# Kernel optimization log

Hardware: AMD Instinct MI355X
Metric: run time of the kernel (lower is better)

## Reference

```python
import jax, jax.numpy as jnp
import numpy as np

N = 50000   # nodes
E = 800000  # edges (avg degree 16)
IN = 128    # in_dim
R = 4       # rank
CMB = 64    # combine_dim
H = 4       # heads
D = 64      # hidden_dim per head
NEG_SLOPE = 0.2


def setup_inputs() -> dict:
    key = jax.random.key(0)
    ks = iter(jax.random.split(key, 24))
    def rnd(shape, s):
        return jax.random.normal(next(ks), shape, jnp.float32) * s
    src = jax.random.randint(next(ks), (E,), 0, N, jnp.int32)
    dst = jax.random.randint(next(ks), (E,), 0, N, jnp.int32)
    ones = jnp.ones((N, 1), jnp.float32)
    # buffers built in __init__: features with a trailing ones column
    h_common = jnp.concatenate([rnd((N, IN), 1.0), ones], axis=-1)      # (N, 129)
    h_type = jnp.concatenate([rnd((N, 512), 1.0), ones], axis=-1)       # (N, 513)
    h_rel = jnp.concatenate([rnd((N, 512), 1.0), ones], axis=-1)        # (N, 513)
    return {
        'src': src, 'dst': dst,
        'h_common': h_common, 'h_type': h_type, 'h_rel': h_rel,
        'Wc': rnd((R, IN + 1, CMB), 0.05),
        'Wt': rnd((R, 513, CMB), 0.05),
        'Wr': rnd((R, 513, CMB), 0.05),
        'fw': rnd((1, R), 0.5),
        'fb': rnd((1, CMB), 0.1),
        'W0': rnd((CMB, H * D), 0.05),
        'al0': rnd((H, D), 0.05), 'ar0': rnd((H, D), 0.05),
        'b0': rnd((H * D,), 0.05),
        'W1': rnd((H * D, H * D), 0.05),
        'al1': rnd((H, D), 0.05), 'ar1': rnd((H, D), 0.05),
        'b1': rnd((H * D,), 0.05),
    }


def _gat_layer(h, src, dst, W, al, ar, b, residual):
    # h: (N, F_in) -> out: (N, H*D), attention a: (E, H)
    feat = (h @ W).reshape(N, H, D)
    el = jnp.einsum('nhd,hd->nh', feat, al)  # (N, H)
    er = jnp.einsum('nhd,hd->nh', feat, ar)
    e = jax.nn.leaky_relu(el[src] + er[dst], NEG_SLOPE)  # (E, H)
    # edge softmax over incoming edges of each dst node
    m = jax.ops.segment_max(e, dst, num_segments=N)      # (N, H)
    ee = jnp.exp(e - m[dst])
    s = jax.ops.segment_sum(ee, dst, num_segments=N)
    a = ee / s[dst]                                       # (E, H)
    msg = feat[src] * a[:, :, None]                       # (E, H, D)
    out = jax.ops.segment_sum(msg, dst, num_segments=N)   # (N, H, D)
    if residual:
        out = out + h.reshape(N, H, D)
    out = out + b.reshape(1, H, D)
    return out.reshape(N, H * D), a


def reference(src, dst, h_common, h_type, h_rel, Wc, Wt, Wr, fw, fb,
              W0, al0, ar0, b0, W1, al1, ar1, b1):
    # low-rank trilinear fusion
    fc = jnp.einsum('ni,ric->rnc', h_common, Wc)  # (R, N, CMB)
    ft = jnp.einsum('ni,ric->rnc', h_type, Wt)
    fr = jnp.einsum('ni,ric->rnc', h_rel, Wr)
    zy = fc * ft * fr
    h = jnp.einsum('r,rnc->nc', fw[0], zy) + fb   # (N, CMB)
    h = jax.nn.elu(h)
    # stacked GAT layers
    h, att = _gat_layer(h, src, dst, W0, al0, ar0, b0, residual=False)
    h, att = _gat_layer(h, src, dst, W1, al1, ar1, b1, residual=True)
    return h, att
```

## Files before the change

kernel.cpp:

```cpp
#include <hip/hip_runtime.h>
#include <math.h>

#define NN 50000
#define EE 800000
#define NEG 0.2f
#define NG (NN / 16)

using f32x4  = __attribute__((ext_vector_type(4))) float;
using bf16x8 = __attribute__((ext_vector_type(8))) short;

__device__ __forceinline__ float lrelu(float x){ return x > 0.f ? x : NEG*x; }

__device__ __forceinline__ unsigned short f2b(float f){
    unsigned int u = __float_as_uint(f);
    return (unsigned short)((u + 0x7FFFu + ((u >> 16) & 1u)) >> 16);
}
__device__ __forceinline__ float b2f(unsigned short h){
    return __uint_as_float(((unsigned int)h) << 16);
}
__device__ __forceinline__ void gld_lds16(const void* g, void* l){
    __builtin_amdgcn_global_load_lds(
        (const __attribute__((address_space(1))) unsigned int*)g,
        (__attribute__((address_space(3))) unsigned int*)l, 16, 0, 0);
}

__global__ void pack_w_fusion(const float* __restrict__ W, unsigned short* __restrict__ out,
                              int K, int NKC)
{
    int u = blockIdx.x * blockDim.x + threadIdx.x;
    if (u >= NKC * 16 * 64) return;
    int l = u & 63, chunk = (u >> 6) & 15, kc = u >> 10;
    int ct = chunk >> 2, r = chunk & 3;
    int c = ct * 16 + (l & 15);
    int kb = kc * 32 + (l >> 4) * 8;
    bf16x8 v;
#pragma unroll
    for (int j = 0; j < 8; ++j)
        v[j] = (short)f2b(W[((size_t)r * K + kb + j) * 64 + c]);
    *(bf16x8*)(out + (size_t)u * 8) = v;
}

template<int PERM>
__global__ void pack_w_gemm(const float* __restrict__ W, unsigned short* __restrict__ out,
                            int K, int C)
{
    int NCH = C / 16;
    int total = (K / 32) * NCH * 64;
    int u = blockIdx.x * blockDim.x + threadIdx.x;
    if (u >= total) return;
    int l = u & 63, ch = (u >> 6) % NCH, kc = u / (64 * NCH);
    int c = ch * 16 + (l & 15);
    int kb = kc * 32 + (l >> 4) * 8;
    bf16x8 v;
#pragma unroll
    for (int j = 0; j < 8; ++j) {
        int k = kb + j;
        int ko = PERM ? ((k & 3) * 64 + (k >> 2)) : k;
        v[j] = (short)f2b(W[(size_t)ko * C + c]);
    }
    *(bf16x8*)(out + (size_t)u * 8) = v;
}

template<int KT, int NKC>
__global__ __launch_bounds__(256) void pack_a_tile(
    const float* __restrict__ F, unsigned short* __restrict__ out)
{
    constexpr int TILES = NKC / 4;
    __shared__ float sf[16][130];
    const int tid = threadIdx.x;
    const int g = blockIdx.x / TILES, t = blockIdx.x % TILES;
    const int nb = g * 16, k0 = t * 128;

#pragma unroll
    for (int i = 0; i < 8; ++i) {
        int idx = tid + i * 256;
        int row = idx >> 7, k = idx & 127;
        sf[row][k] = F[(size_t)(nb + row) * KT + k0 + k];
    }
    __syncthreads();
    {
        int kcl = tid >> 6, l = tid & 63;
        int row = l & 15, kb = kcl * 32 + (l >> 4) * 8;
        bf16x8 o;
#pragma unroll
        for (int j = 0; j < 8; ++j) o[j] = (short)f2b(sf[row][kb + j]);
        *(bf16x8*)(out + ((size_t)(g * NKC + t * 4 + kcl) * 64 + l) * 8) = o;
    }
}

template<int NKC>
__device__ __forceinline__ void fusion_pass_lds(
    const unsigned short* __restrict__ ldsA, int cbase,
    const unsigned short* __restrict__ wp,
    const float* __restrict__ W, int K, int w, int l, f32x4 (&acc)[4])
{
    const int c_lo = l & 15;
#pragma unroll
    for (int ct = 0; ct < 4; ++ct) {
        float wi = W[((size_t)w * K + (K - 1)) * 64 + ct * 16 + c_lo];
        acc[ct] = f32x4{wi, wi, wi, wi};
    }
#pragma unroll
    for (int kc = 0; kc < NKC; ++kc) {
        bf16x8 af = *(const bf16x8*)(ldsA + (cbase + kc) * 512 + l * 8);
        const unsigned short* wk = wp + (size_t)kc * 8192 + w * 512 + l * 8;
#pragma unroll
        for (int ct = 0; ct < 4; ++ct) {
            bf16x8 bf = *(const bf16x8*)(wk + ct * 2048);
            acc[ct] = __builtin_amdgcn_mfma_f32_16x16x32_bf16(af, bf, acc[ct], 0, 0, 0);
        }
    }
}

__global__ __launch_bounds__(256) void fusion_mfma(
    const unsigned short* __restrict__ apc, const unsigned short* __restrict__ apt,
    const unsigned short* __restrict__ apr,
    const unsigned short* __restrict__ wpc, const unsigned short* __restrict__ wpt,
    const unsigned short* __restrict__ wpr,
    const float* __restrict__ Wc, const float* __restrict__ Wt, const float* __restrict__ Wr,
    const float* __restrict__ fw, const float* __restrict__ fb,
    unsigned short* __restrict__ h0b)
{
    __shared__ __align__(16) char smem[36864];
    unsigned short* ldsA = (unsigned short*)smem;
    float* ldsx = (float*)smem;
    const int w = threadIdx.x >> 6, l = threadIdx.x & 63;
    const int G = blockIdx.x;

#pragma unroll
    for (int j = 0; j < 9; ++j) {
        int cid = w * 9 + j;
        const unsigned short* s;
        if (cid < 4)       s = apc + ((size_t)G * 4  + cid) * 512;
        else if (cid < 20) s = apt + ((size_t)G * 16 + (cid - 4)) * 512;
        else               s = apr + ((size_t)G * 16 + (cid - 20)) * 512;
        gld_lds16(s + l * 8, ldsA + cid * 512);
    }
    __syncthreads();

    f32x4 prod[4], acc[4];
    fusion_pass_lds<4>(ldsA, 0, wpc, Wc, 129, w, l, acc);
#pragma unroll
    for (int ct = 0; ct < 4; ++ct) prod[ct] = acc[ct];
    fusion_pass_lds<16>(ldsA, 4, wpt, Wt, 513, w, l, acc);
#pragma unroll
    for (int ct = 0; ct < 4; ++ct) prod[ct] *= acc[ct];
    fusion_pass_lds<16>(ldsA, 20, wpr, Wr, 513, w, l, acc);
    const float fww = fw[w];
#pragma unroll
    for (int ct = 0; ct < 4; ++ct) prod[ct] = prod[ct] * acc[ct] * fww;

    __syncthreads();
#pragma unroll
    for (int ct = 0; ct < 4; ++ct)
        *(f32x4*)&ldsx[((w * 4 + ct) * 64 + l) * 4] = prod[ct];
    __syncthreads();

    f32x4 s = *(const f32x4*)&ldsx[((0 * 4 + w) * 64 + l) * 4];
#pragma unroll
    for (int r = 1; r < 4; ++r)
        s += *(const f32x4*)&ldsx[((r * 4 + w) * 64 + l) * 4];

    const int c = w * 16 + (l & 15);
    const float fbc = fb[c];
#pragma unroll
    for (int q = 0; q < 4; ++q) {
        int n = G * 16 + (l >> 4) * 4 + q;
        float v = s[q] + fbc;
        v = v > 0.f ? v : expm1f(v);
        h0b[(size_t)n * 64 + c] = f2b(v);
    }
}

template<int K>
__global__ __launch_bounds__(256) void gemm_reg(
    const unsigned short* __restrict__ Ab, const unsigned short* __restrict__ wp,
    const float* __restrict__ al, const float* __restrict__ ar,
    unsigned short* __restrict__ featb,
    float* __restrict__ el, float* __restrict__ er)
{
    constexpr int NKC = K / 32;
    const int w = threadIdx.x >> 6, l = threadIdx.x & 63;
    const int nb = blockIdx.x * 16;

    f32x4 acc[4];
#pragma unroll
    for (int i = 0; i < 4; ++i) acc[i] = f32x4{0.f, 0.f, 0.f, 0.f};

    const unsigned short* abase = Ab + (size_t)(nb + (l & 15)) * K + (l >> 4) * 8;
    bf16x8 afs[NKC];
#pragma unroll
    for (int kc = 0; kc < NKC; ++kc)
        afs[kc] = *(const bf16x8*)(abase + kc * 32);

    bf16x8 bcur[4];
    {
        const unsigned short* wk = wp + (size_t)(0 * 16 + w * 4) * 512 + l * 8;
#pragma unroll
        for (int i = 0; i < 4; ++i) bcur[i] = *(const bf16x8*)(wk + i * 512);
    }
#pragma unroll
    for (int kc = 0; kc < NKC; ++kc) {
        bf16x8 bnxt[4];
        if (kc + 1 < NKC) {
            const unsigned short* wk = wp + ((size_t)(kc + 1) * 16 + w * 4) * 512 + l * 8;
#pragma unroll
            for (int i = 0; i < 4; ++i) bnxt[i] = *(const bf16x8*)(wk + i * 512);
        }
#pragma unroll
        for (int i = 0; i < 4; ++i)
            acc[i] = __builtin_amdgcn_mfma_f32_16x16x32_bf16(afs[kc], bcur[i], acc[i], 0, 0, 0);
        if (kc + 1 < NKC) {
#pragma unroll
            for (int i = 0; i < 4; ++i) bcur[i] = bnxt[i];
        }
    }

#pragma unroll
    for (int i = 0; i < 4; ++i) {
        int c = (w * 4 + i) * 16 + (l & 15);
        int dm = (c & 63) * 4 + (c >> 6);
#pragma unroll
        for (int q = 0; q < 4; ++q) {
            int n = nb + (l >> 4) * 4 + q;
            featb[(size_t)n * 256 + dm] = f2b(acc[i][q]);
        }
    }

    float pel[4] = {0.f, 0.f, 0.f, 0.f};
    float per_[4] = {0.f, 0.f, 0.f, 0.f};
#pragma unroll
    for (int i = 0; i < 4; ++i) {
        int d = i * 16 + (l & 15);
        float av = al[w * 64 + d];
        float rv = ar[w * 64 + d];
#pragma unroll
        for (int q = 0; q < 4; ++q) {
            pel[q] += acc[i][q] * av;
            per_[q] += acc[i][q] * rv;
        }
    }
#pragma unroll
    for (int off = 1; off <= 8; off <<= 1) {
#pragma unroll
        for (int q = 0; q < 4; ++q) {
            pel[q] += __shfl_xor(pel[q], off);
            per_[q] += __shfl_xor(per_[q], off);
        }
    }
    int qsel = l & 15;
    if (qsel < 4) {
        float ev = qsel == 0 ? pel[0] : qsel == 1 ? pel[1] : qsel == 2 ? pel[2] : pel[3];
        float rv = qsel == 0 ? per_[0] : qsel == 1 ? per_[1] : qsel == 2 ? per_[2] : per_[3];
        int n = nb + (l >> 4) * 4 + qsel;
        el[(size_t)n * 4 + w] = ev;
        er[(size_t)n * 4 + w] = rv;
    }
}

__global__ void hist_kernel(const int* __restrict__ dst, int* __restrict__ cnt)
{
    int e = blockIdx.x * blockDim.x + threadIdx.x;
    if (e < EE) atomicAdd(&cnt[dst[e]], 1);
}

__global__ __launch_bounds__(1024) void scan_kernel(const int* __restrict__ cnt, int* __restrict__ offs)
{
    __shared__ int tmp[1024];
    const int t = threadIdx.x;
    const int C = (NN + 1023) / 1024;
    int lo = t * C, hi = min(lo + C, NN);
    int s = 0;
    for (int i = lo; i < hi; ++i) s += cnt[i];
    tmp[t] = s;
    __syncthreads();
    for (int off = 1; off < 1024; off <<= 1) {
        int v = (t >= off) ? tmp[t - off] : 0;
        __syncthreads();
        tmp[t] += v;
        __syncthreads();
    }
    int run = (t == 0) ? 0 : tmp[t - 1];
    for (int i = lo; i < hi; ++i) { offs[i] = run; run += cnt[i]; }
    if (t == 1023) offs[NN] = tmp[1023];
}

__global__ void scatter_kernel(const int* __restrict__ dst, const int* __restrict__ offs,
                               int* __restrict__ cur, int* __restrict__ esort)
{
    int e = blockIdx.x * blockDim.x + threadIdx.x;
    if (e < EE) {
        int d = dst[e];
        int p = offs[d] + atomicAdd(&cur[d], 1);
        esort[p] = e;
    }
}

__global__ void edge_prep(const int* __restrict__ esort, const int* __restrict__ src,
                          const int* __restrict__ dst,
                          const float* __restrict__ el, const float* __restrict__ er,
                          float4* __restrict__ eesort, int* __restrict__ srcsort)
{
    int p = blockIdx.x * blockDim.x + threadIdx.x;
    if (p >= EE) return;
    int e = esort[p];
    int s = src[e], d = dst[e];
    srcsort[p] = s;
    float4 l4 = *(const float4*)(el + (size_t)s * 4);
    float4 r4 = *(const float4*)(er + (size_t)d * 4);
    eesort[p] = make_float4(lrelu(l4.x + r4.x), lrelu(l4.y + r4.y),
                            lrelu(l4.z + r4.z), lrelu(l4.w + r4.w));
}

template <int RESID, int WMZ, int WB16, int WF32>
__global__ __launch_bounds__(256) void gat_agg(
    const int* __restrict__ srcsort, const int* __restrict__ offs,
    const unsigned short* __restrict__ featb, float4* __restrict__ eesort,
    const unsigned short* __restrict__ residb, const float* __restrict__ bias,
    float* __restrict__ out, unsigned short* __restrict__ outb,
    float4* __restrict__ mbuf, float4* __restrict__ zbuf)
{
    int n = (int)((blockIdx.x * (size_t)blockDim.x + threadIdx.x) >> 6);
    int lane = threadIdx.x & 63;
    if (n >= NN) return;
    int s0 = offs[n], s1 = offs[n + 1];

    float m0 = -1e30f, m1 = -1e30f, m2 = -1e30f, m3 = -1e30f;
    for (int p = s0 + lane; p < s1; p += 64) {
        float4 v = eesort[p];
        m0 = fmaxf(m0, v.x); m1 = fmaxf(m1, v.y);
        m2 = fmaxf(m2, v.z); m3 = fmaxf(m3, v.w);
    }
#pragma unroll
    for (int off = 32; off; off >>= 1) {
        m0 = fmaxf(m0, __shfl_xor(m0, off));
        m1 = fmaxf(m1, __shfl_xor(m1, off));
        m2 = fmaxf(m2, __shfl_xor(m2, off));
        m3 = fmaxf(m3, __shfl_xor(m3, off));
    }

    float z0 = 0.f, z1 = 0.f, z2 = 0.f, z3 = 0.f;
    for (int p = s0 + lane; p < s1; p += 64) {
        float4 v = eesort[p];
        v.x = expf(v.x - m0); v.y = expf(v.y - m1);
        v.z = expf(v.z - m2); v.w = expf(v.w - m3);
        eesort[p] = v;
        z0 += v.x; z1 += v.y; z2 += v.z; z3 += v.w;
    }
    __threadfence_block();
#pragma unroll
    for (int off = 32; off; off >>= 1) {
        z0 += __shfl_xor(z0, off);
        z1 += __shfl_xor(z1, off);
        z2 += __shfl_xor(z2, off);
        z3 += __shfl_xor(z3, off);
    }
    float i0 = z0 > 0.f ? 1.f / z0 : 0.f;
    float i1 = z1 > 0.f ? 1.f / z1 : 0.f;
    float i2 = z2 > 0.f ? 1.f / z2 : 0.f;
    float i3 = z3 > 0.f ? 1.f / z3 : 0.f;
    if (WMZ && lane == 0) {
        mbuf[n] = make_float4(m0, m1, m2, m3);
        zbuf[n] = make_float4(i0, i1, i2, i3);
    }

    float a0 = 0.f, a1 = 0.f, a2 = 0.f, a3 = 0.f;
    float c0 = 0.f, c1 = 0.f, c2 = 0.f, c3 = 0.f;
    int p = s0;
    for (; p + 3 < s1; p += 4) {
        float4 wA = eesort[p],     wB = eesort[p + 1];
        float4 wC = eesort[p + 2], wD = eesort[p + 3];
        int sA = srcsort[p],     sB = srcsort[p + 1];
        int sC = srcsort[p + 2], sD = srcsort[p + 3];
        ushort4 fA = *(const ushort4*)(featb + (size_t)sA * 256 + lane * 4);
        ushort4 fB = *(const ushort4*)(featb + (size_t)sB * 256 + lane * 4);
        ushort4 fC = *(const ushort4*)(featb + (size_t)sC * 256 + lane * 4);
        ushort4 fD = *(const ushort4*)(featb + (size_t)sD * 256 + lane * 4);
        a0 += wA.x * b2f(fA.x);  c0 += wB.x * b2f(fB.x);
        a1 += wA.y * b2f(fA.y);  c1 += wB.y * b2f(fB.y);
        a2 += wA.z * b2f(fA.z);  c2 += wB.z * b2f(fB.z);
        a3 += wA.w * b2f(fA.w);  c3 += wB.w * b2f(fB.w);
        a0 += wC.x * b2f(fC.x);  c0 += wD.x * b2f(fD.x);
        a1 += wC.y * b2f(fC.y);  c1 += wD.y * b2f(fD.y);
        a2 += wC.z * b2f(fC.z);  c2 += wD.z * b2f(fD.z);
        a3 += wC.w * b2f(fC.w);  c3 += wD.w * b2f(fD.w);
    }
    for (; p < s1; ++p) {
        float4 wA = eesort[p];
        int sA = srcsort[p];
        ushort4 fA = *(const ushort4*)(featb + (size_t)sA * 256 + lane * 4);
        a0 += wA.x * b2f(fA.x);
        a1 += wA.y * b2f(fA.y);
        a2 += wA.z * b2f(fA.z);
        a3 += wA.w * b2f(fA.w);
    }
    a0 += c0; a1 += c1; a2 += c2; a3 += c3;

    float o0 = a0 * i0 + bias[lane];
    float o1 = a1 * i1 + bias[64 + lane];
    float o2 = a2 * i2 + bias[128 + lane];
    float o3 = a3 * i3 + bias[192 + lane];
    if (RESID) {
        ushort4 rp = *(const ushort4*)(residb + (size_t)n * 256 + lane * 4);
        o0 += b2f(rp.x); o1 += b2f(rp.y); o2 += b2f(rp.z); o3 += b2f(rp.w);
    }
    if (WF32) {
        float* op = out + (size_t)n * 256;
        op[lane] = o0;
        op[64 + lane] = o1;
        op[128 + lane] = o2;
        op[192 + lane] = o3;
    }
    if (WB16) {
        ushort4 ob;
        ob.x = f2b(o0); ob.y = f2b(o1); ob.z = f2b(o2); ob.w = f2b(o3);
        *(ushort4*)(outb + (size_t)n * 256 + lane * 4) = ob;
    }
}

__global__ void att_final(const int* __restrict__ src, const int* __restrict__ dst,
                          const float* __restrict__ el, const float* __restrict__ er,
                          const float4* __restrict__ mbuf, const float4* __restrict__ zbuf,
                          float4* __restrict__ att)
{
    int e = blockIdx.x * blockDim.x + threadIdx.x;
    if (e >= EE) return;
    int s = src[e], d = dst[e];
    float4 l4 = *(const float4*)(el + (size_t)s * 4);
    float4 r4 = *(const float4*)(er + (size_t)d * 4);
    float4 m4 = mbuf[d], zi = zbuf[d];
    att[e] = make_float4(expf(lrelu(l4.x + r4.x) - m4.x) * zi.x,
                         expf(lrelu(l4.y + r4.y) - m4.y) * zi.y,
                         expf(lrelu(l4.z + r4.z) - m4.z) * zi.z,
                         expf(lrelu(l4.w + r4.w) - m4.w) * zi.w);
}

extern "C" void kernel_launch(void* const* d_in, const int* in_sizes, int n_in,
                              void* d_out, int out_size, void* d_ws, size_t ws_size,
                              hipStream_t stream)
{
    const int*   src = (const int*)d_in[0];
    const int*   dst = (const int*)d_in[1];
    const float* hc  = (const float*)d_in[2];
    const float* ht  = (const float*)d_in[3];
    const float* hr  = (const float*)d_in[4];
    const float* Wc  = (const float*)d_in[5];
    const float* Wt  = (const float*)d_in[6];
    const float* Wr  = (const float*)d_in[7];
    const float* fw  = (const float*)d_in[8];
    const float* fb  = (const float*)d_in[9];
    const float* W0  = (const float*)d_in[10];
    const float* al0 = (const float*)d_in[11];
    const float* ar0 = (const float*)d_in[12];
    const float* b0  = (const float*)d_in[13];
    const float* W1  = (const float*)d_in[14];
    const float* al1 = (const float*)d_in[15];
    const float* ar1 = (const float*)d_in[16];
    const float* b1  = (const float*)d_in[17];

    char* ws = (char*)d_ws;
    unsigned short* h0b   = (unsigned short*)(ws);
    unsigned short* h1b   = (unsigned short*)(ws + 6400000);
    unsigned short* featb = (unsigned short*)(ws + 32000000);
    float* el    = (float*)(ws + 57600000);
    float* er    = (float*)(ws + 58400000);
    int*   cnt   = (int*)  (ws + 59200000);
    int*   offs  = (int*)  (ws + 59400000);
    int*   esort = (int*)  (ws + 59600128);
    unsigned short* wpc = (unsigned short*)(ws + 62800128);
    unsigned short* wpt = (unsigned short*)(ws + 62865664);
    unsigned short* wpr = (unsigned short*)(ws + 63127808);
    unsigned short* wp0 = (unsigned short*)(ws + 63389952);
    unsigned short* wp1 = (unsigned short*)(ws + 63422720);
    float4* mbuf = (float4*)(ws + 63553792);
    float4* zbuf = (float4*)(ws + 64353792);
    int* srcsort = (int*)  (ws + 65153792);
    if (ws_size < 68353792ull) return;

    float* outh = (float*)d_out;
    float4* atto = (float4*)(outh + (size_t)NN * 256);

    unsigned short* apt = (unsigned short*)d_out;
    unsigned short* apc = (unsigned short*)((char*)d_out + 51200000);
    unsigned short* apr = (unsigned short*)(ws + 6400000);

    pack_w_fusion<<<(4 * 16 * 64 + 255) / 256, 256, 0, stream>>>(Wc, wpc, 129, 4);
    pack_w_fusion<<<(16 * 16 * 64 + 255) / 256, 256, 0, stream>>>(Wt, wpt, 513, 16);
    pack_w_fusion<<<(16 * 16 * 64 + 255) / 256, 256, 0, stream>>>(Wr, wpr, 513, 16);
    pack_w_gemm<0><<<(2 * 16 * 64 + 255) / 256, 256, 0, stream>>>(W0, wp0, 64, 256);
    pack_w_gemm<1><<<(8 * 16 * 64 + 255) / 256, 256, 0, stream>>>(W1, wp1, 256, 256);

    pack_a_tile<129, 4><<<NG * 1, 256, 0, stream>>>(hc, apc);
    pack_a_tile<513, 16><<<NG * 4, 256, 0, stream>>>(ht, apt);
    pack_a_tile<513, 16><<<NG * 4, 256, 0, stream>>>(hr, apr);

    fusion_mfma<<<NG, 256, 0, stream>>>(apc, apt, apr, wpc, wpt, wpr,
                                        Wc, Wt, Wr, fw, fb, h0b);

    hipMemsetAsync(cnt, 0, NN * sizeof(int), stream);
    hist_kernel<<<(EE + 255) / 256, 256, 0, stream>>>(dst, cnt);
    scan_kernel<<<1, 1024, 0, stream>>>(cnt, offs);
    hipMemsetAsync(cnt, 0, NN * sizeof(int), stream);
    scatter_kernel<<<(EE + 255) / 256, 256, 0, stream>>>(dst, offs, cnt, esort);

    gemm_reg<64><<<NG, 256, 0, stream>>>(h0b, wp0, al0, ar0, featb, el, er);
    edge_prep<<<(EE + 255) / 256, 256, 0, stream>>>(esort, src, dst, el, er, atto, srcsort);
    gat_agg<0, 0, 1, 0><<<(NN * 64 + 255) / 256, 256, 0, stream>>>(
        srcsort, offs, featb, atto, nullptr, b0, nullptr, h1b, nullptr, nullptr);

    gemm_reg<256><<<NG, 256, 0, stream>>>(h1b, wp1, al1, ar1, featb, el, er);
    edge_prep<<<(EE + 255) / 256, 256, 0, stream>>>(esort, src, dst, el, er, atto, srcsort);
    gat_agg<1, 1, 0, 1><<<(NN * 64 + 255) / 256, 256, 0, stream>>>(
        srcsort, offs, featb, atto, h1b, b1, outh, nullptr, mbuf, zbuf);
    att_final<<<(EE + 255) / 256, 256, 0, stream>>>(src, dst, el, er, mbuf, zbuf, atto);
}
```

Baseline: 571.8 us.

## Fuse edge score, softmax and attention output into GAT aggregation kernel

Removes the separate edge_prep and att_final kernels and computes edge scores directly inside gat_agg from el/er. For nodes with degree up to 64, each lane holds one edge's weights in registers, softmax reductions use wave shuffles, and the normalized weights are broadcast by shuffle during aggregation. Attention is written straight from the aggregation kernel. This cuts the sorted score and source buffers, their round trips through memory, and three launches. In exchange, the unrolled 4-edge aggregation loop becomes a serial shuffle loop, and high-degree nodes recompute scores three times with extra indirect loads.

```diff
diff --git a/kernel.cpp b/kernel.cpp
--- a/kernel.cpp
+++ b/kernel.cpp
@@ -296,105 +296,127 @@
     }
 }
 
-__global__ void edge_prep(const int* __restrict__ esort, const int* __restrict__ src,
-                          const int* __restrict__ dst,
-                          const float* __restrict__ el, const float* __restrict__ er,
-                          float4* __restrict__ eesort, int* __restrict__ srcsort)
-{
-    int p = blockIdx.x * blockDim.x + threadIdx.x;
-    if (p >= EE) return;
-    int e = esort[p];
-    int s = src[e], d = dst[e];
-    srcsort[p] = s;
-    float4 l4 = *(const float4*)(el + (size_t)s * 4);
-    float4 r4 = *(const float4*)(er + (size_t)d * 4);
-    eesort[p] = make_float4(lrelu(l4.x + r4.x), lrelu(l4.y + r4.y),
-                            lrelu(l4.z + r4.z), lrelu(l4.w + r4.w));
-}
-
-template <int RESID, int WMZ, int WB16, int WF32>
+template <int RESID, int WATT, int WB16, int WF32>
 __global__ __launch_bounds__(256) void gat_agg(
-    const int* __restrict__ srcsort, const int* __restrict__ offs,
-    const unsigned short* __restrict__ featb, float4* __restrict__ eesort,
+    const int* __restrict__ esort, const int* __restrict__ src, const int* __restrict__ offs,
+    const unsigned short* __restrict__ featb,
+    const float* __restrict__ el, const float* __restrict__ er,
     const unsigned short* __restrict__ residb, const float* __restrict__ bias,
     float* __restrict__ out, unsigned short* __restrict__ outb,
-    float4* __restrict__ mbuf, float4* __restrict__ zbuf)
+    float4* __restrict__ att)
 {
     int n = (int)((blockIdx.x * (size_t)blockDim.x + threadIdx.x) >> 6);
     int lane = threadIdx.x & 63;
     if (n >= NN) return;
-    int s0 = offs[n], s1 = offs[n + 1];
-
-    float m0 = -1e30f, m1 = -1e30f, m2 = -1e30f, m3 = -1e30f;
-    for (int p = s0 + lane; p < s1; p += 64) {
-        float4 v = eesort[p];
-        m0 = fmaxf(m0, v.x); m1 = fmaxf(m1, v.y);
-        m2 = fmaxf(m2, v.z); m3 = fmaxf(m3, v.w);
-    }
-#pragma unroll
-    for (int off = 32; off; off >>= 1) {
-        m0 = fmaxf(m0, __shfl_xor(m0, off));
-        m1 = fmaxf(m1, __shfl_xor(m1, off));
-        m2 = fmaxf(m2, __shfl_xor(m2, off));
-        m3 = fmaxf(m3, __shfl_xor(m3, off));
-    }
-
-    float z0 = 0.f, z1 = 0.f, z2 = 0.f, z3 = 0.f;
-    for (int p = s0 + lane; p < s1; p += 64) {
-        float4 v = eesort[p];
-        v.x = expf(v.x - m0); v.y = expf(v.y - m1);
-        v.z = expf(v.z - m2); v.w = expf(v.w - m3);
-        eesort[p] = v;
-        z0 += v.x; z1 += v.y; z2 += v.z; z3 += v.w;
-    }
-    __threadfence_block();
-#pragma unroll
-    for (int off = 32; off; off >>= 1) {
-        z0 += __shfl_xor(z0, off);
-        z1 += __shfl_xor(z1, off);
-        z2 += __shfl_xor(z2, off);
-        z3 += __shfl_xor(z3, off);
-    }
-    float i0 = z0 > 0.f ? 1.f / z0 : 0.f;
-    float i1 = z1 > 0.f ? 1.f / z1 : 0.f;
-    float i2 = z2 > 0.f ? 1.f / z2 : 0.f;
-    float i3 = z3 > 0.f ? 1.f / z3 : 0.f;
-    if (WMZ && lane == 0) {
-        mbuf[n] = make_float4(m0, m1, m2, m3);
-        zbuf[n] = make_float4(i0, i1, i2, i3);
-    }
+    const int s0 = offs[n], s1 = offs[n + 1], deg = s1 - s0;
+    const float4 r4 = *(const float4*)(er + (size_t)n * 4);
 
     float a0 = 0.f, a1 = 0.f, a2 = 0.f, a3 = 0.f;
-    float c0 = 0.f, c1 = 0.f, c2 = 0.f, c3 = 0.f;
-    int p = s0;
-    for (; p + 3 < s1; p += 4) {
-        float4 wA = eesort[p],     wB = eesort[p + 1];
-        float4 wC = eesort[p + 2], wD = eesort[p + 3];
-        int sA = srcsort[p],     sB = srcsort[p + 1];
-        int sC = srcsort[p + 2], sD = srcsort[p + 3];
-        ushort4 fA = *(const ushort4*)(featb + (size_t)sA * 256 + lane * 4);
-        ushort4 fB = *(const ushort4*)(featb + (size_t)sB * 256 + lane * 4);
-        ushort4 fC = *(const ushort4*)(featb + (size_t)sC * 256 + lane * 4);
-        ushort4 fD = *(const ushort4*)(featb + (size_t)sD * 256 + lane * 4);
-        a0 += wA.x * b2f(fA.x);  c0 += wB.x * b2f(fB.x);
-        a1 += wA.y * b2f(fA.y);  c1 += wB.y * b2f(fB.y);
-        a2 += wA.z * b2f(fA.z);  c2 += wB.z * b2f(fB.z);
-        a3 += wA.w * b2f(fA.w);  c3 += wB.w * b2f(fB.w);
-        a0 += wC.x * b2f(fC.x);  c0 += wD.x * b2f(fD.x);
-        a1 += wC.y * b2f(fC.y);  c1 += wD.y * b2f(fD.y);
-        a2 += wC.z * b2f(fC.z);  c2 += wD.z * b2f(fD.z);
-        a3 += wC.w * b2f(fC.w);  c3 += wD.w * b2f(fD.w);
-    }
-    for (; p < s1; ++p) {
-        float4 wA = eesort[p];
-        int sA = srcsort[p];
-        ushort4 fA = *(const ushort4*)(featb + (size_t)sA * 256 + lane * 4);
-        a0 += wA.x * b2f(fA.x);
-        a1 += wA.y * b2f(fA.y);
-        a2 += wA.z * b2f(fA.z);
-        a3 += wA.w * b2f(fA.w);
-    }
-    a0 += c0; a1 += c1; a2 += c2; a3 += c3;
+    float i0, i1, i2, i3;
+
+    if (deg <= 64) {
+        int p = s0 + lane;
+        bool valid = p < s1;
+        int e = valid ? esort[p] : 0;
+        int sv = valid ? src[e] : 0;
+        float v0 = -1e30f, v1 = -1e30f, v2 = -1e30f, v3 = -1e30f;
+        if (valid) {
+            float4 l4 = *(const float4*)(el + (size_t)sv * 4);
+            v0 = lrelu(l4.x + r4.x); v1 = lrelu(l4.y + r4.y);
+            v2 = lrelu(l4.z + r4.z); v3 = lrelu(l4.w + r4.w);
+        }
+        float m0 = v0, m1 = v1, m2 = v2, m3 = v3;
+#pragma unroll
+        for (int off = 32; off; off >>= 1) {
+            m0 = fmaxf(m0, __shfl_xor(m0, off));
+            m1 = fmaxf(m1, __shfl_xor(m1, off));
+            m2 = fmaxf(m2, __shfl_xor(m2, off));
+            m3 = fmaxf(m3, __shfl_xor(m3, off));
+        }
+        float e0 = valid ? expf(v0 - m0) : 0.f;
+        float e1 = valid ? expf(v1 - m1) : 0.f;
+        float e2 = valid ? expf(v2 - m2) : 0.f;
+        float e3 = valid ? expf(v3 - m3) : 0.f;
+        float z0 = e0, z1 = e1, z2 = e2, z3 = e3;
+#pragma unroll
+        for (int off = 32; off; off >>= 1) {
+            z0 += __shfl_xor(z0, off);
+            z1 += __shfl_xor(z1, off);
+            z2 += __shfl_xor(z2, off);
+            z3 += __shfl_xor(z3, off);
+        }
+        float j0 = z0 > 0.f ? 1.f / z0 : 0.f;
+        float j1 = z1 > 0.f ? 1.f / z1 : 0.f;
+        float j2 = z2 > 0.f ? 1.f / z2 : 0.f;
+        float j3 = z3 > 0.f ? 1.f / z3 : 0.f;
+        e0 *= j0; e1 *= j1; e2 *= j2; e3 *= j3;
+        if (WATT && valid)
+            att[e] = make_float4(e0, e1, e2, e3);
+        for (int jj = 0; jj < deg; ++jj) {
+            float w0 = __shfl(e0, jj), w1 = __shfl(e1, jj);
+            float w2 = __shfl(e2, jj), w3 = __shfl(e3, jj);
+            int s = __shfl(sv, jj);
+            ushort4 f = *(const ushort4*)(featb + (size_t)s * 256 + lane * 4);
+            a0 += w0 * b2f(f.x);
+            a1 += w1 * b2f(f.y);
+            a2 += w2 * b2f(f.z);
+            a3 += w3 * b2f(f.w);
+        }
+        i0 = i1 = i2 = i3 = 1.f;
+    } else {
+        float m0 = -1e30f, m1 = -1e30f, m2 = -1e30f, m3 = -1e30f;
+        for (int p = s0 + lane; p < s1; p += 64) {
+            int s = src[esort[p]];
+            float4 l4 = *(const float4*)(el + (size_t)s * 4);
+            m0 = fmaxf(m0, lrelu(l4.x + r4.x));
+            m1 = fmaxf(m1, lrelu(l4.y + r4.y));
+            m2 = fmaxf(m2, lrelu(l4.z + r4.z));
+            m3 = fmaxf(m3, lrelu(l4.w + r4.w));
+        }
+#pragma unroll
+        for (int off = 32; off; off >>= 1) {
+            m0 = fmaxf(m0, __shfl_xor(m0, off));
+            m1 = fmaxf(m1, __shfl_xor(m1, off));
+            m2 = fmaxf(m2, __shfl_xor(m2, off));
+            m3 = fmaxf(m3, __shfl_xor(m3, off));
+        }
+        float z0 = 0.f, z1 = 0.f, z2 = 0.f, z3 = 0.f;
+        for (int p = s0 + lane; p < s1; p += 64) {
+            int s = src[esort[p]];
+            float4 l4 = *(const float4*)(el + (size_t)s * 4);
+            z0 += expf(lrelu(l4.x + r4.x) - m0);
+            z1 += expf(lrelu(l4.y + r4.y) - m1);
+            z2 += expf(lrelu(l4.z + r4.z) - m2);
+            z3 += expf(lrelu(l4.w + r4.w) - m3);
+        }
+#pragma unroll
+        for (int off = 32; off; off >>= 1) {
+            z0 += __shfl_xor(z0, off);
+            z1 += __shfl_xor(z1, off);
+            z2 += __shfl_xor(z2, off);
+            z3 += __shfl_xor(z3, off);
+        }
+        i0 = z0 > 0.f ? 1.f / z0 : 0.f;
+        i1 = z1 > 0.f ? 1.f / z1 : 0.f;
+        i2 = z2 > 0.f ? 1.f / z2 : 0.f;
+        i3 = z3 > 0.f ? 1.f / z3 : 0.f;
+        for (int p = s0; p < s1; ++p) {
+            int e = esort[p];
+            int s = src[e];
+            float4 l4 = *(const float4*)(el + (size_t)s * 4);
+            float w0 = expf(lrelu(l4.x + r4.x) - m0);
+            float w1 = expf(lrelu(l4.y + r4.y) - m1);
+            float w2 = expf(lrelu(l4.z + r4.z) - m2);
+            float w3 = expf(lrelu(l4.w + r4.w) - m3);
+            ushort4 f = *(const ushort4*)(featb + (size_t)s * 256 + lane * 4);
+            a0 += w0 * b2f(f.x);
+            a1 += w1 * b2f(f.y);
+            a2 += w2 * b2f(f.z);
+            a3 += w3 * b2f(f.w);
+            if (WATT && lane == 0)
+                att[e] = make_float4(w0 * i0, w1 * i1, w2 * i2, w3 * i3);
+        }
+    }
 
     float o0 = a0 * i0 + bias[lane];
     float o1 = a1 * i1 + bias[64 + lane];
@@ -416,23 +438,6 @@
         ob.x = f2b(o0); ob.y = f2b(o1); ob.z = f2b(o2); ob.w = f2b(o3);
         *(ushort4*)(outb + (size_t)n * 256 + lane * 4) = ob;
     }
-}
-
-__global__ void att_final(const int* __restrict__ src, const int* __restrict__ dst,
-                          const float* __restrict__ el, const float* __restrict__ er,
-                          const float4* __restrict__ mbuf, const float4* __restrict__ zbuf,
-                          float4* __restrict__ att)
-{
-    int e = blockIdx.x * blockDim.x + threadIdx.x;
-    if (e >= EE) return;
-    int s = src[e], d = dst[e];
-    float4 l4 = *(const float4*)(el + (size_t)s * 4);
-    float4 r4 = *(const float4*)(er + (size_t)d * 4);
-    float4 m4 = mbuf[d], zi = zbuf[d];
-    att[e] = make_float4(expf(lrelu(l4.x + r4.x) - m4.x) * zi.x,
-                         expf(lrelu(l4.y + r4.y) - m4.y) * zi.y,
-                         expf(lrelu(l4.z + r4.z) - m4.z) * zi.z,
-                         expf(lrelu(l4.w + r4.w) - m4.w) * zi.w);
 }
 
 extern "C" void kernel_launch(void* const* d_in, const int* in_sizes, int n_in,
@@ -472,10 +477,7 @@
     unsigned short* wpr = (unsigned short*)(ws + 63127808);
     unsigned short* wp0 = (unsigned short*)(ws + 63389952);
     unsigned short* wp1 = (unsigned short*)(ws + 63422720);
-    float4* mbuf = (float4*)(ws + 63553792);
-    float4* zbuf = (float4*)(ws + 64353792);
-    int* srcsort = (int*)  (ws + 65153792);
-    if (ws_size < 68353792ull) return;
+    if (ws_size < 63553792ull) return;
 
     float* outh = (float*)d_out;
     float4* atto = (float4*)(outh + (size_t)NN * 256);
@@ -504,13 +506,10 @@
     scatter_kernel<<<(EE + 255) / 256, 256, 0, stream>>>(dst, offs, cnt, esort);
 
     gemm_reg<64><<<NG, 256, 0, stream>>>(h0b, wp0, al0, ar0, featb, el, er);
-    edge_prep<<<(EE + 255) / 256, 256, 0, stream>>>(esort, src, dst, el, er, atto, srcsort);
     gat_agg<0, 0, 1, 0><<<(NN * 64 + 255) / 256, 256, 0, stream>>>(
-        srcsort, offs, featb, atto, nullptr, b0, nullptr, h1b, nullptr, nullptr);
+        esort, src, offs, featb, el, er, nullptr, b0, nullptr, h1b, nullptr);
 
     gemm_reg<256><<<NG, 256, 0, stream>>>(h1b, wp1, al1, ar1, featb, el, er);
-    edge_prep<<<(EE + 255) / 256, 256, 0, stream>>>(esort, src, dst, el, er, atto, srcsort);
     gat_agg<1, 1, 0, 1><<<(NN * 64 + 255) / 256, 256, 0, stream>>>(
-        srcsort, offs, featb, atto, h1b, b1, outh, nullptr, mbuf, zbuf);
-    att_final<<<(EE + 255) / 256, 256, 0, stream>>>(src, dst, el, er, mbuf, zbuf, atto);
-}
+        esort, src, offs, featb, el, er, h1b, b1, outh, nullptr, atto);
+}
```

Result: faster. 548.9 us (-4.0%).
